# Kernel optimization log

Measured on AMD Instinct MI355X. Metric: run time of the kernel, lower is better.

## Reference

```python
import jax, jax.numpy as jnp
import numpy as np

H = 512  # hidden_dimension
B = 32
S = 2048


def setup_inputs() -> dict:
    key = jax.random.key(0)
    k1, k2, k3, k4, k5, k6 = jax.random.split(key, 6)
    decoder_hide = jax.random.normal(k1, (B, H), dtype=jnp.float32)
    encoder_out = jax.random.normal(k2, (B, S, 2 * H), dtype=jnp.float32)
    mask = jax.random.randint(k3, (B, S), 0, 2, dtype=jnp.int32)
    bound = 1.0 / np.sqrt(3 * H)
    W_attn = jax.random.uniform(k4, (3 * H, H), minval=-bound, maxval=bound, dtype=jnp.float32)
    b_attn = jax.random.uniform(k5, (H,), minval=-bound, maxval=bound, dtype=jnp.float32)
    bound_v = 1.0 / np.sqrt(H)
    v_w = jax.random.uniform(k6, (H,), minval=-bound_v, maxval=bound_v, dtype=jnp.float32)
    return {"decoder_hide": decoder_hide, "encoder_out": encoder_out, "mask": mask,
            "W_attn": W_attn, "b_attn": b_attn, "v_w": v_w}


def reference(decoder_hide, encoder_out, mask, W_attn, b_attn, v_w):
    # Split the concat-linear: cat((h, enc)) @ W == h @ W[:H] + enc @ W[H:]
    W_h = W_attn[:H]        # [H, H]
    W_e = W_attn[H:]        # [2H, H]
    dec_proj = decoder_hide @ W_h + b_attn                 # [B, H]
    enc_proj = jnp.einsum('bse,eh->bsh', encoder_out, W_e)  # [B, S, H]
    energy = jnp.tanh(enc_proj + dec_proj[:, None, :])      # [B, S, H]
    attention = jnp.einsum('bsh,h->bs', energy, v_w)        # [B, S]
    attention = jnp.where(mask == 0, jnp.float32(-100000.0), attention)
    return jax.nn.softmax(attention, axis=1)
```

## Files before the change

### kernel.cpp

```cpp
#include <hip/hip_runtime.h>
#include <hip/hip_bf16.h>
#include <math.h>

#define Hdim 512
#define Bdim 32
#define Sdim 2048
#define Kdim 1024
#define Mtot (Bdim * Sdim)

#define BM 128
#define BK 64

typedef __attribute__((ext_vector_type(8))) short short8;
typedef __attribute__((ext_vector_type(4))) float floatx4;

__device__ __forceinline__ short f2bf(float f) {
    union { float f; unsigned u; } v; v.f = f;
    unsigned r = v.u + 0x7fffu + ((v.u >> 16) & 1u);
    return (short)(r >> 16);
}

__device__ __forceinline__ short8 cvt8(float4 a, float4 b) {
    union { short8 s; __hip_bfloat162 h[4]; } u;
    u.h[0] = __float22bfloat162_rn(make_float2(a.x, a.y));
    u.h[1] = __float22bfloat162_rn(make_float2(a.z, a.w));
    u.h[2] = __float22bfloat162_rn(make_float2(b.x, b.y));
    u.h[3] = __float22bfloat162_rn(make_float2(b.z, b.w));
    return u.s;
}

__device__ __forceinline__ float fast_tanh(float x) {
    float ax = fabsf(x);
    float e  = __expf(-2.0f * ax);
    float r  = (1.0f - e) * __builtin_amdgcn_rcpf(1.0f + e);
    return copysignf(r, x);
}

__global__ __launch_bounds__(256) void prep_kernel(
    const float* __restrict__ W_attn, const float* __restrict__ dec,
    const float* __restrict__ b_attn, short* __restrict__ Wbp,
    float* __restrict__ dec_proj)
{
    const int t = threadIdx.x;
    if (blockIdx.x < 512) {
        const float* We = W_attn + Hdim * Hdim;
        __shared__ short tile[32][33];
        const int k0 = (blockIdx.x >> 4) * 32;
        const int n0 = (blockIdx.x & 15) * 32;
        const int r = t >> 5, c = t & 31;
        #pragma unroll
        for (int rr = 0; rr < 4; ++rr)
            tile[r + rr * 8][c] = f2bf(We[(size_t)(k0 + r + rr * 8) * Hdim + n0 + c]);
        __syncthreads();
        if (t < 128) {
            const int n_loc = t >> 2;
            const int q     = t & 3;
            const int nt    = (n0 + n_loc) >> 4;
            const int lnn   = (n0 + n_loc) & 15;
            const int ks    = k0 >> 5;
            short8 v;
            #pragma unroll
            for (int r2 = 0; r2 < 8; ++r2) v[r2] = tile[q * 8 + r2][n_loc];
            ((short8*)Wbp)[((nt * 32 + ks) * 64) + q * 16 + lnn] = v;
        }
    } else {
        __shared__ float partl[2][128];
        const int bid = blockIdx.x - 512;
        const int b  = bid >> 2;
        const int cb = bid & 3;
        const int c  = cb * 128 + (t & 127);
        const int kh = t >> 7;
        float acc = 0.0f;
        const int kbeg = kh * 256, kend = kbeg + 256;
        #pragma unroll 8
        for (int k = kbeg; k < kend; ++k)
            acc = fmaf(dec[b * Hdim + k], W_attn[(size_t)k * Hdim + c], acc);
        partl[kh][t & 127] = acc;
        __syncthreads();
        if (t < 128)
            dec_proj[b * Hdim + cb * 128 + t] = partl[0][t] + partl[1][t] + b_attn[cb * 128 + t];
    }
}

__device__ __forceinline__ void kstep(
    int kt, short* __restrict__ Ab, float4& ra, float4& rb,
    const float* __restrict__ Ag, const short8* __restrict__ Bp,
    int w, int abase, int pf0, int pf1, int awo,
    floatx4 (&acc)[8][2])
{
    const size_t ks = (size_t)(kt >> 5);
    const size_t nt0 = (size_t)(w * 2 + 0) * 32;
    const size_t nt1 = (size_t)(w * 2 + 1) * 32;
    short8 b0[2], b1[2];
    b0[0] = Bp[(nt0 + ks) * 64];
    b0[1] = Bp[(nt1 + ks) * 64];
    b1[0] = Bp[(nt0 + ks + 1) * 64];
    b1[1] = Bp[(nt1 + ks + 1) * 64];

    *(short8*)&Ab[awo] = cvt8(ra, rb);
    __syncthreads();

    if (kt + 2 * BK < Kdim) {
        const float4* g = (const float4*)(Ag + kt + 2 * BK);
        ra = g[0]; rb = g[1];
    }

    short8 af[4];
    #pragma unroll
    for (int i2 = 0; i2 < 4; ++i2)
        af[i2] = *(const short8*)&Ab[abase + i2 * 1024 + pf0];
    #pragma unroll
    for (int i2 = 0; i2 < 4; ++i2)
        #pragma unroll
        for (int j = 0; j < 2; ++j)
            acc[i2][j] = __builtin_amdgcn_mfma_f32_16x16x32_bf16(
                             af[i2], b0[j], acc[i2][j], 0, 0, 0);
    #pragma unroll
    for (int i2 = 0; i2 < 4; ++i2)
        af[i2] = *(const short8*)&Ab[abase + (i2 + 4) * 1024 + pf0];
    #pragma unroll
    for (int i2 = 0; i2 < 4; ++i2)
        #pragma unroll
        for (int j = 0; j < 2; ++j)
            acc[i2 + 4][j] = __builtin_amdgcn_mfma_f32_16x16x32_bf16(
                                 af[i2], b0[j], acc[i2 + 4][j], 0, 0, 0);
    #pragma unroll
    for (int i2 = 0; i2 < 4; ++i2)
        af[i2] = *(const short8*)&Ab[abase + i2 * 1024 + pf1];
    #pragma unroll
    for (int i2 = 0; i2 < 4; ++i2)
        #pragma unroll
        for (int j = 0; j < 2; ++j)
            acc[i2][j] = __builtin_amdgcn_mfma_f32_16x16x32_bf16(
                             af[i2], b1[j], acc[i2][j], 0, 0, 0);
    #pragma unroll
    for (int i2 = 0; i2 < 4; ++i2)
        af[i2] = *(const short8*)&Ab[abase + (i2 + 4) * 1024 + pf1];
    #pragma unroll
    for (int i2 = 0; i2 < 4; ++i2)
        #pragma unroll
        for (int j = 0; j < 2; ++j)
            acc[i2 + 4][j] = __builtin_amdgcn_mfma_f32_16x16x32_bf16(
                                 af[i2], b1[j], acc[i2 + 4][j], 0, 0, 0);
}

__global__ __launch_bounds__(1024, 4) void scores_kernel(
    const float* __restrict__ enc,
    const short* __restrict__ Wbp,
    const float* __restrict__ dec_proj,
    const float* __restrict__ v_w,
    float* __restrict__ scores)
{
    __shared__ __align__(16) short Asm[2 * BM * BK];
    __shared__ float redl[BM][16];

    const int t    = threadIdx.x;
    const int row0 = blockIdx.x * BM;
    const int b    = row0 / Sdim;

    const int w    = t >> 6;
    const int lane = t & 63;
    const int ln   = lane & 15;
    const int quad = lane >> 4;

    const int sm = t >> 3;
    const int sq = t & 7;
    const float* Ag = enc + (size_t)(row0 + sm) * Kdim + sq * 8;
    const int awo = sm * BK + ((sq ^ (sm & 7)) * 8);

    const int abase = ln * BK;
    const int pf0 = (quad ^ (ln & 7)) * 8;
    const int pf1 = pf0 ^ 32;

    const short8* Bp = ((const short8*)Wbp) + lane;

    floatx4 acc[8][2];
    #pragma unroll
    for (int i = 0; i < 8; ++i)
        #pragma unroll
        for (int j = 0; j < 2; ++j)
            acc[i][j] = (floatx4)(0.0f);

    float4 r0a, r0b, r1a, r1b;
    { const float4* g = (const float4*)Ag;        r0a = g[0]; r0b = g[1]; }
    { const float4* g = (const float4*)(Ag + BK); r1a = g[0]; r1b = g[1]; }

    for (int kt = 0; kt < Kdim; kt += 2 * BK) {
        kstep(kt,      Asm,           r0a, r0b, Ag, Bp, w, abase, pf0, pf1, awo, acc);
        kstep(kt + BK, Asm + BM * BK, r1a, r1b, Ag, Bp, w, abase, pf0, pf1, awo, acc);
    }

    float dpv[2], vwv[2];
    #pragma unroll
    for (int j = 0; j < 2; ++j) {
        const int col = w * 32 + j * 16 + ln;
        dpv[j] = dec_proj[b * Hdim + col];
        vwv[j] = v_w[col];
    }
    #pragma unroll
    for (int i = 0; i < 8; ++i) {
        #pragma unroll
        for (int reg = 0; reg < 4; ++reg) {
            float s = 0.0f;
            #pragma unroll
            for (int j = 0; j < 2; ++j) {
                float x = acc[i][j][reg] + dpv[j];
                s = fmaf(vwv[j], fast_tanh(x), s);
            }
            s += __shfl_xor(s, 1, 64);
            s += __shfl_xor(s, 2, 64);
            s += __shfl_xor(s, 4, 64);
            s += __shfl_xor(s, 8, 64);
            if (ln == 0)
                redl[i * 16 + quad * 4 + reg][w] = s;
        }
    }
    __syncthreads();
    if (t < BM) {
        float s = 0.0f;
        #pragma unroll
        for (int wv = 0; wv < 16; ++wv) s += redl[t][wv];
        scores[row0 + t] = s;
    }
}

__global__ __launch_bounds__(256) void softmax_kernel(
    const float* __restrict__ scores, const int* __restrict__ mask,
    float* __restrict__ out)
{
    __shared__ float sred[8];
    const int b = blockIdx.x;
    const int t = threadIdx.x;
    const int lane = t & 63;
    const int wid  = t >> 6;

    float x[8];
    float m = -1e30f;
    #pragma unroll
    for (int j = 0; j < 8; ++j) {
        int idx = b * Sdim + j * 256 + t;
        float v = scores[idx];
        if (mask[idx] == 0) v = -100000.0f;
        x[j] = v;
        m = fmaxf(m, v);
    }
    #pragma unroll
    for (int off = 32; off >= 1; off >>= 1)
        m = fmaxf(m, __shfl_xor(m, off, 64));
    if (lane == 0) sred[wid] = m;
    __syncthreads();
    m = fmaxf(fmaxf(sred[0], sred[1]), fmaxf(sred[2], sred[3]));

    float s = 0.0f;
    #pragma unroll
    for (int j = 0; j < 8; ++j) {
        float e = __expf(x[j] - m);
        x[j] = e;
        s += e;
    }
    #pragma unroll
    for (int off = 32; off >= 1; off >>= 1)
        s += __shfl_xor(s, off, 64);
    if (lane == 0) sred[4 + wid] = s;
    __syncthreads();
    s = sred[4] + sred[5] + sred[6] + sred[7];

    const float inv = 1.0f / s;
    #pragma unroll
    for (int j = 0; j < 8; ++j)
        out[b * Sdim + j * 256 + t] = x[j] * inv;
}

extern "C" void kernel_launch(void* const* d_in, const int* in_sizes, int n_in,
                              void* d_out, int out_size, void* d_ws, size_t ws_size,
                              hipStream_t stream) {
    const float* dec  = (const float*)d_in[0];
    const float* enc  = (const float*)d_in[1];
    const int*   mask = (const int*)  d_in[2];
    const float* W    = (const float*)d_in[3];
    const float* ba   = (const float*)d_in[4];
    const float* vw   = (const float*)d_in[5];
    float* out = (float*)d_out;

    float* dec_proj = (float*)d_ws;
    short* Wbp      = (short*)(dec_proj + Bdim * Hdim);
    float* scores   = (float*)(Wbp + Hdim * Kdim);

    prep_kernel<<<640, 256, 0, stream>>>(W, dec, ba, Wbp, dec_proj);
    scores_kernel<<<Mtot / BM, 1024, 0, stream>>>(enc, Wbp, dec_proj, vw, scores);
    softmax_kernel<<<Bdim, 256, 0, stream>>>(scores, mask, out);
}
```

Before: 445.4 us.

## Halve scores block to 8 waves, each computing 64 output columns

```diff
diff --git a/kernel.cpp b/kernel.cpp
--- a/kernel.cpp
+++ b/kernel.cpp
@@ -83,26 +83,27 @@
 }
 
 __device__ __forceinline__ void kstep(
-    int kt, short* __restrict__ Ab, float4& ra, float4& rb,
+    int kt, short* __restrict__ Ab, float4 (&ra)[4],
     const float* __restrict__ Ag, const short8* __restrict__ Bp,
-    int w, int abase, int pf0, int pf1, int awo,
-    floatx4 (&acc)[8][2])
+    int w, int abase, int pf0, int pf1, int awo0, int awo1,
+    floatx4 (&acc)[8][4])
 {
     const size_t ks = (size_t)(kt >> 5);
-    const size_t nt0 = (size_t)(w * 2 + 0) * 32;
-    const size_t nt1 = (size_t)(w * 2 + 1) * 32;
-    short8 b0[2], b1[2];
-    b0[0] = Bp[(nt0 + ks) * 64];
-    b0[1] = Bp[(nt1 + ks) * 64];
-    b1[0] = Bp[(nt0 + ks + 1) * 64];
-    b1[1] = Bp[(nt1 + ks + 1) * 64];
-
-    *(short8*)&Ab[awo] = cvt8(ra, rb);
-    __syncthreads();
-
-    if (kt + 2 * BK < Kdim) {
-        const float4* g = (const float4*)(Ag + kt + 2 * BK);
-        ra = g[0]; rb = g[1];
+    short8 b0[4], b1[4];
+    #pragma unroll
+    for (int j = 0; j < 4; ++j)
+        b0[j] = Bp[((size_t)(w * 4 + j) * 32 + ks) * 64];
+    #pragma unroll
+    for (int j = 0; j < 4; ++j)
+        b1[j] = Bp[((size_t)(w * 4 + j) * 32 + ks + 1) * 64];
+
+    *(short8*)&Ab[awo0] = cvt8(ra[0], ra[1]);
+    *(short8*)&Ab[awo1] = cvt8(ra[2], ra[3]);
+    __syncthreads();
+
+    if (kt + BK < Kdim) {
+        const float4* g = (const float4*)(Ag + kt + BK);
+        ra[0] = g[0]; ra[1] = g[1]; ra[2] = g[2]; ra[3] = g[3];
     }
 
     short8 af[4];
@@ -112,7 +113,7 @@
     #pragma unroll
     for (int i2 = 0; i2 < 4; ++i2)
         #pragma unroll
-        for (int j = 0; j < 2; ++j)
+        for (int j = 0; j < 4; ++j)
             acc[i2][j] = __builtin_amdgcn_mfma_f32_16x16x32_bf16(
                              af[i2], b0[j], acc[i2][j], 0, 0, 0);
     #pragma unroll
@@ -121,7 +122,7 @@
     #pragma unroll
     for (int i2 = 0; i2 < 4; ++i2)
         #pragma unroll
-        for (int j = 0; j < 2; ++j)
+        for (int j = 0; j < 4; ++j)
             acc[i2 + 4][j] = __builtin_amdgcn_mfma_f32_16x16x32_bf16(
                                  af[i2], b0[j], acc[i2 + 4][j], 0, 0, 0);
     #pragma unroll
@@ -130,7 +131,7 @@
     #pragma unroll
     for (int i2 = 0; i2 < 4; ++i2)
         #pragma unroll
-        for (int j = 0; j < 2; ++j)
+        for (int j = 0; j < 4; ++j)
             acc[i2][j] = __builtin_amdgcn_mfma_f32_16x16x32_bf16(
                              af[i2], b1[j], acc[i2][j], 0, 0, 0);
     #pragma unroll
@@ -139,12 +140,12 @@
     #pragma unroll
     for (int i2 = 0; i2 < 4; ++i2)
         #pragma unroll
-        for (int j = 0; j < 2; ++j)
+        for (int j = 0; j < 4; ++j)
             acc[i2 + 4][j] = __builtin_amdgcn_mfma_f32_16x16x32_bf16(
                                  af[i2], b1[j], acc[i2 + 4][j], 0, 0, 0);
 }
 
-__global__ __launch_bounds__(1024, 4) void scores_kernel(
+__global__ __launch_bounds__(512, 2) void scores_kernel(
     const float* __restrict__ enc,
     const short* __restrict__ Wbp,
     const float* __restrict__ dec_proj,
@@ -152,7 +153,7 @@
     float* __restrict__ scores)
 {
     __shared__ __align__(16) short Asm[2 * BM * BK];
-    __shared__ float redl[BM][16];
+    __shared__ float redl[BM][9];
 
     const int t    = threadIdx.x;
     const int row0 = blockIdx.x * BM;
@@ -163,10 +164,11 @@
     const int ln   = lane & 15;
     const int quad = lane >> 4;
 
-    const int sm = t >> 3;
-    const int sq = t & 7;
-    const float* Ag = enc + (size_t)(row0 + sm) * Kdim + sq * 8;
-    const int awo = sm * BK + ((sq ^ (sm & 7)) * 8);
+    const int sm  = t >> 2;
+    const int sqb = (t & 3) * 2;
+    const float* Ag = enc + (size_t)(row0 + sm) * Kdim + sqb * 8;
+    const int awo0 = sm * BK + ((sqb       ^ (sm & 7)) * 8);
+    const int awo1 = sm * BK + (((sqb + 1) ^ (sm & 7)) * 8);
 
     const int abase = ln * BK;
     const int pf0 = (quad ^ (ln & 7)) * 8;
@@ -174,26 +176,26 @@
 
     const short8* Bp = ((const short8*)Wbp) + lane;
 
-    floatx4 acc[8][2];
+    floatx4 acc[8][4];
     #pragma unroll
     for (int i = 0; i < 8; ++i)
         #pragma unroll
-        for (int j = 0; j < 2; ++j)
+        for (int j = 0; j < 4; ++j)
             acc[i][j] = (floatx4)(0.0f);
 
-    float4 r0a, r0b, r1a, r1b;
-    { const float4* g = (const float4*)Ag;        r0a = g[0]; r0b = g[1]; }
-    { const float4* g = (const float4*)(Ag + BK); r1a = g[0]; r1b = g[1]; }
-
+    float4 ra[4];
+    { const float4* g = (const float4*)Ag; ra[0] = g[0]; ra[1] = g[1]; ra[2] = g[2]; ra[3] = g[3]; }
+
+    #pragma unroll 1
     for (int kt = 0; kt < Kdim; kt += 2 * BK) {
-        kstep(kt,      Asm,           r0a, r0b, Ag, Bp, w, abase, pf0, pf1, awo, acc);
-        kstep(kt + BK, Asm + BM * BK, r1a, r1b, Ag, Bp, w, abase, pf0, pf1, awo, acc);
-    }
-
-    float dpv[2], vwv[2];
-    #pragma unroll
-    for (int j = 0; j < 2; ++j) {
-        const int col = w * 32 + j * 16 + ln;
+        kstep(kt,      Asm,           ra, Ag, Bp, w, abase, pf0, pf1, awo0, awo1, acc);
+        kstep(kt + BK, Asm + BM * BK, ra, Ag, Bp, w, abase, pf0, pf1, awo0, awo1, acc);
+    }
+
+    float dpv[4], vwv[4];
+    #pragma unroll
+    for (int j = 0; j < 4; ++j) {
+        const int col = w * 64 + j * 16 + ln;
         dpv[j] = dec_proj[b * Hdim + col];
         vwv[j] = v_w[col];
     }
@@ -203,7 +205,7 @@
         for (int reg = 0; reg < 4; ++reg) {
             float s = 0.0f;
             #pragma unroll
-            for (int j = 0; j < 2; ++j) {
+            for (int j = 0; j < 4; ++j) {
                 float x = acc[i][j][reg] + dpv[j];
                 s = fmaf(vwv[j], fast_tanh(x), s);
             }
@@ -219,7 +221,7 @@
     if (t < BM) {
         float s = 0.0f;
         #pragma unroll
-        for (int wv = 0; wv < 16; ++wv) s += redl[t][wv];
+        for (int wv = 0; wv < 8; ++wv) s += redl[t][wv];
         scores[row0 + t] = s;
     }
 }
@@ -287,6 +289,6 @@
     float* scores   = (float*)(Wbp + Hdim * Kdim);
 
     prep_kernel<<<640, 256, 0, stream>>>(W, dec, ba, Wbp, dec_proj);
-    scores_kernel<<<Mtot / BM, 1024, 0, stream>>>(enc, Wbp, dec_proj, vw, scores);
+    scores_kernel<<<Mtot / BM, 512, 0, stream>>>(enc, Wbp, dec_proj, vw, scores);
     softmax_kernel<<<Bdim, 256, 0, stream>>>(scores, mask, out);
 }
```

Result: faster. 427.5 us (-4.0%).
